# Kernel optimization log

Hardware: AMD Instinct MI355X
Metric: run time of the kernel (lower is better)

The kernel has to match this reference:

```python
import jax, jax.numpy as jnp
import numpy as np
from jax import lax

PAIRS = ((0, 1), (1, 2), (2, 3), (3, 0))


def _apply_1q(state, U, w):
    # state: (N,2,2,2,2); wire w lives at axis w+1
    state = jnp.moveaxis(state, w + 1, -1)
    if U.ndim == 2:  # shared gate across batch
        state = jnp.einsum('ij,...j->...i', U, state)
    else:            # per-batch gate (encoder), U: (N,2,2)
        state = jnp.einsum('nij,n...j->n...i', U, state)
    return jnp.moveaxis(state, -1, w + 1)


def _ry_mat(theta):
    # torchquantum RY: [[cos(t/2), -sin(t/2)], [sin(t/2), cos(t/2)]]
    h = theta * 0.5
    c, s = jnp.cos(h), jnp.sin(h)
    return jnp.stack([jnp.stack([c, -s], -1), jnp.stack([s, c], -1)], -2).astype(jnp.complex64)


def _rz_mat(theta):
    # torchquantum RZ: diag(e^{-i t/2}, e^{+i t/2})
    h = (theta * 0.5).astype(jnp.complex64)
    e0, e1 = jnp.exp(-1j * h), jnp.exp(1j * h)
    z = jnp.zeros_like(e0)
    return jnp.stack([jnp.stack([e0, z], -1), jnp.stack([z, e1], -1)], -2)


def _cnot(state, c, t):
    st = jnp.moveaxis(state, (c + 1, t + 1), (-2, -1))
    st = jnp.stack([st[..., 0, :], st[..., 1, ::-1]], axis=-2)
    return jnp.moveaxis(st, (-2, -1), (c + 1, t + 1))


def _ansatz(state, p, a, b):
    state = _apply_1q(state, _ry_mat(p[0]), a)
    state = _apply_1q(state, _rz_mat(p[1]), a)
    state = _apply_1q(state, _ry_mat(p[2]), b)
    state = _apply_1q(state, _rz_mat(p[3]), b)
    state = _cnot(state, a, b)
    state = _apply_1q(state, _ry_mat(p[4]), a)
    state = _apply_1q(state, _rz_mat(p[5]), a)
    state = _apply_1q(state, _ry_mat(p[6]), b)
    return state


def _circuit(angles, qp):
    # angles: (N,4) in [0,pi]; qp: (2,7). Returns <Z_w> per wire: (N,4)
    N = angles.shape[0]
    state = jnp.zeros((N, 2, 2, 2, 2), jnp.complex64).at[:, 0, 0, 0, 0].set(1.0)
    for w in range(4):  # GeneralEncoder: RY(x_w) on wire w
        state = _apply_1q(state, _ry_mat(angles[:, w]), w)
    for layer in range(2):
        for (a, b) in PAIRS:
            state = _ansatz(state, qp[layer], a, b)
    probs = state.real ** 2 + state.imag ** 2
    exps = []
    for w in range(4):
        axes = tuple(ax for ax in range(1, 5) if ax != w + 1)
        m = probs.sum(axis=axes)  # (N,2)
        exps.append(m[:, 0] - m[:, 1])
    return jnp.stack(exps, axis=-1)


def _conv(x, w, b):
    y = lax.conv_general_dilated(x, w, (1, 1), 'SAME',
                                 dimension_numbers=('NCHW', 'OIHW', 'NCHW'))
    return y + b[None, :, None, None]


def _pool(x):
    return lax.reduce_window(x, -jnp.inf, lax.max, (1, 1, 2, 2), (1, 1, 2, 2), 'VALID')


def setup_inputs() -> dict:
    key = jax.random.key(0)
    ks = jax.random.split(key, 16)
    r = lambda k, sh, sc=0.1: (jax.random.normal(k, sh, dtype=jnp.float32) * sc)
    return {
        'x': jax.random.normal(ks[0], (2048, 1, 28, 28), dtype=jnp.float32),
        'conv1_w': r(ks[1], (64, 1, 3, 3)), 'conv1_b': r(ks[2], (64,)),
        'conv2_w': r(ks[3], (16, 64, 3, 3)), 'conv2_b': r(ks[4], (16,)),
        'conv3_w': r(ks[5], (4, 16, 3, 3)), 'conv3_b': r(ks[6], (4,)),
        'q_params': jax.random.uniform(ks[7], (2, 7), dtype=jnp.float32),
        'fc1_w': r(ks[8], (64, 196)), 'fc1_b': r(ks[9], (64,)),
        'fc2_w': r(ks[10], (128, 64)), 'fc2_b': r(ks[11], (128,)),
        'fc3_w': r(ks[12], (64, 128)), 'fc3_b': r(ks[13], (64,)),
        'fc4_w': r(ks[14], (10, 64)), 'fc4_b': r(ks[15], (10,)),
    }


def reference(x, conv1_w, conv1_b, conv2_w, conv2_b, conv3_w, conv3_b,
              q_params, fc1_w, fc1_b, fc2_w, fc2_b, fc3_w, fc3_b, fc4_w, fc4_b):
    h = _pool(jax.nn.relu(_conv(x, conv1_w, conv1_b)))       # (B,64,14,14)
    h = _pool(jax.nn.relu(_conv(h, conv2_w, conv2_b)))       # (B,16,7,7)
    h = jax.nn.leaky_relu(_conv(h, conv3_w, conv3_b), 0.01)  # (B,4,7,7)
    B, C, H, W = h.shape
    # 1x1 patches: (B, H*W, C) -> flatten over patches
    patches = h.reshape(B, C, H * W).transpose(0, 2, 1).reshape(B * H * W, C)
    angles = jax.nn.sigmoid(patches) * np.float32(np.pi)
    q = _circuit(angles, q_params)            # (B*49, 4)
    q = q.reshape(B, H * W * C)               # (B, 196)
    h = jax.nn.relu(q @ fc1_w.T + fc1_b)
    h = h @ fc2_w.T + fc2_b
    h = jax.nn.relu(h @ fc3_w.T + fc3_b)
    return h @ fc4_w.T + fc4_b
```

## Files before the change

### kernel.cpp

```cpp
#include <hip/hip_runtime.h>
#include <hip/hip_bf16.h>
#include <math.h>

#define DEV __device__ __forceinline__

typedef __attribute__((ext_vector_type(4))) float f32x4;
typedef __attribute__((ext_vector_type(8))) short bf16x8;

DEV unsigned short f2bf(float v) {
    __hip_bfloat16 h = __float2bfloat16(v);
    return *reinterpret_cast<unsigned short*>(&h);
}
DEV unsigned pk2(float a, float b) {
    union { __hip_bfloat162 b2; unsigned u; } cv;
    cv.b2 = __float22bfloat162_rn(float2{a, b});
    return cv.u;
}

template<int B>
DEV void ry_b(float* sr, float* si, float c, float s) {
    #pragma unroll
    for (int i = 0; i < 16; ++i) if (!(i & B)) {
        int j = i | B;
        float r0 = sr[i], m0 = si[i], r1 = sr[j], m1 = si[j];
        sr[i] = c * r0 - s * r1;  si[i] = c * m0 - s * m1;
        sr[j] = s * r0 + c * r1;  si[j] = s * m0 + c * m1;
    }
}
template<int B>
DEV void rz_b(float* sr, float* si, float c, float s) {
    #pragma unroll
    for (int i = 0; i < 16; ++i) {
        float xr = sr[i], xi = si[i];
        if (!(i & B)) { sr[i] = c * xr + s * xi;  si[i] = c * xi - s * xr; }
        else          { sr[i] = c * xr - s * xi;  si[i] = c * xi + s * xr; }
    }
}
template<int BC, int BT>
DEV void cnot_b(float* sr, float* si) {
    #pragma unroll
    for (int i = 0; i < 16; ++i) if ((i & BC) && !(i & BT)) {
        int j = i | BT;
        float tr = sr[i]; sr[i] = sr[j]; sr[j] = tr;
        float ti = si[i]; si[i] = si[j]; si[j] = ti;
    }
}
template<int A, int Bw>
DEV void ansatz(float* sr, float* si, const float* cc, const float* ss) {
    constexpr int BA = 8 >> A, BB = 8 >> Bw;
    ry_b<BA>(sr, si, cc[0], ss[0]);
    rz_b<BA>(sr, si, cc[1], ss[1]);
    ry_b<BB>(sr, si, cc[2], ss[2]);
    rz_b<BB>(sr, si, cc[3], ss[3]);
    cnot_b<BA, BB>(sr, si);
    ry_b<BA>(sr, si, cc[4], ss[4]);
    rz_b<BA>(sr, si, cc[5], ss[5]);
    ry_b<BB>(sr, si, cc[6], ss[6]);
}

__global__ void prep_kernel(const float* __restrict__ w1,
                            const float* __restrict__ w2,
                            const float* __restrict__ w3,
                            const float* __restrict__ qp,
                            const float* __restrict__ fc1w,
                            const float* __restrict__ fc2w,
                            const float* __restrict__ fc3w,
                            const float* __restrict__ fc4w,
                            unsigned short* __restrict__ w1b,
                            unsigned short* __restrict__ w2b,
                            float* __restrict__ w3t,
                            float* __restrict__ ab,
                            float* __restrict__ fc1t,
                            float* __restrict__ fc2t,
                            float* __restrict__ fc3t,
                            float* __restrict__ fc4t)
{
    int t = blockIdx.x * blockDim.x + threadIdx.x;
    int NT = gridDim.x * blockDim.x;
    for (int i = t; i < 2048; i += NT) {
        int j = i & 7, oc = (i >> 3) & 63, fqq = i >> 9;
        int tap = fqq * 8 + j;
        w1b[i] = tap < 9 ? f2bf(w1[oc * 9 + tap]) : (unsigned short)0;
    }
    for (int i = t; i < 9216; i += NT) {
        int j = i & 7, oc = (i >> 3) & 15, fq = (i >> 7) & 3, f = i >> 9;
        int tap = f >> 1, kk = f & 1;
        int s = kk * 32 + fq * 8 + j;
        int ic = (s & 3) * 16 + (s >> 2);
        w2b[i] = f2bf(w2[(oc * 64 + ic) * 9 + tap]);
    }
    for (int i = t; i < 576; i += NT) {
        int c = i & 3, ch = (i >> 2) & 15, tap = i >> 6;
        w3t[i] = w3[(c * 16 + ch) * 9 + tap];
    }
    for (int i = t; i < 12544; i += NT) { int j = i / 196, k = i % 196; fc1t[k * 64 + j] = fc1w[i]; }
    for (int i = t; i < 8192;  i += NT) { int j = i / 64,  k = i % 64;  fc2t[k * 128 + j] = fc2w[i]; }
    for (int i = t; i < 8192;  i += NT) { int j = i / 128, k = i % 128; fc3t[k * 64 + j] = fc3w[i]; }
    for (int i = t; i < 640;   i += NT) { int j = i / 64,  k = i % 64;  fc4t[k * 10 + j] = fc4w[i]; }

    if (blockIdx.x == 0 && threadIdx.x < 16) {
        int b = threadIdx.x;
        float cs0[7], sn0[7], cs1[7], sn1[7];
        #pragma unroll
        for (int k = 0; k < 7; ++k) {
            __sincosf(qp[k] * 0.5f, &sn0[k], &cs0[k]);
            __sincosf(qp[7 + k] * 0.5f, &sn1[k], &cs1[k]);
        }
        float sr[16], si[16];
        #pragma unroll
        for (int i = 0; i < 16; ++i) { sr[i] = (i == b) ? 1.f : 0.f; si[i] = 0.f; }
        ansatz<0, 1>(sr, si, cs0, sn0);
        ansatz<1, 2>(sr, si, cs0, sn0);
        ansatz<2, 3>(sr, si, cs0, sn0);
        ansatz<3, 0>(sr, si, cs0, sn0);
        ansatz<0, 1>(sr, si, cs1, sn1);
        ansatz<1, 2>(sr, si, cs1, sn1);
        ansatz<2, 3>(sr, si, cs1, sn1);
        ansatz<3, 0>(sr, si, cs1, sn1);
        #pragma unroll
        for (int i = 0; i < 16; ++i) {
            ab[(i * 16 + b) * 2]     = sr[i];
            ab[(i * 16 + b) * 2 + 1] = si[i];
        }
    }
}

__global__ __launch_bounds__(256, 3) void conv12_kernel(
    const float* __restrict__ x,
    const float* __restrict__ b1, const unsigned short* __restrict__ w1b,
    const unsigned short* __restrict__ w2b,
    const float* __restrict__ b2, float* __restrict__ out2)
{
    __shared__ __align__(128) char lds_all[36864];
    float* pin = (float*)lds_all;
    char* in_b = lds_all + 4096;
    int t = threadIdx.x, lane = t & 63, wv = t >> 6;
    int fq = lane >> 4, fr = lane & 15;
    int n = blockIdx.x;

    bf16x8 bfrag[18];
    const bf16x8* wb = (const bf16x8*)w2b;
    #pragma unroll
    for (int f = 0; f < 18; ++f) bfrag[f] = wb[(f * 4 + fq) * 16 + fr];
    bf16x8 w1f[4];
    const bf16x8* wb1 = (const bf16x8*)w1b;
    float b1v[4];
    #pragma unroll
    for (int nt = 0; nt < 4; ++nt) {
        w1f[nt] = wb1[fq * 64 + nt * 16 + fr];
        b1v[nt] = b1[nt * 16 + fr];
    }
    float b2v = b2[fr];

    for (int i = t; i < 2048; i += 256) ((f32x4*)in_b)[i] = f32x4{0.f, 0.f, 0.f, 0.f};
    for (int i = t; i < 1020; i += 256) pin[i] = 0.f;
    if (t < 128) {
        int cell = t >> 2, comp = t & 3;
        int pos;
        if (cell < 9)       pos = cell;
        else if (cell < 18) pos = 72 + (cell - 9);
        else if (cell < 25) pos = (cell - 17) * 9;
        else                pos = (cell - 24) * 9 + 8;
        *reinterpret_cast<float4*>(out2 + (size_t)n * 1296 + pos * 16 + comp * 4)
            = float4{0.f, 0.f, 0.f, 0.f};
    }
    __syncthreads();
    for (int i = t; i < 784; i += 256) pin[(i / 28 + 1) * 34 + (i % 28) + 1] = x[n * 784 + i];
    __syncthreads();

    for (int tile = wv; tile < 49; tile += 4) {
        int pooledA = tile * 4 + (fr >> 2);
        int pyA = pooledA / 14, pxA = pooledA - pyA * 14;
        int Y = 2 * pyA + ((fr >> 1) & 1), X = 2 * pxA + (fr & 1);
        const float* ap = pin + Y * 34 + X + (fq == 1 ? 70 : 0);
        float q0 = ap[0],  q1 = ap[1],  q2 = ap[2];
        float q3 = ap[34], q4 = ap[35], q5 = ap[36];
        float q6 = ap[68], q7 = ap[69];
        union { uint4 u; bf16x8 v; } A;
        A.u.x = pk2(q0, q1); A.u.y = pk2(q2, q3);
        A.u.z = pk2(q4, q5); A.u.w = pk2(q6, q7);

        f32x4 a0 = {0.f,0.f,0.f,0.f}, a1 = {0.f,0.f,0.f,0.f},
              a2 = {0.f,0.f,0.f,0.f}, a3 = {0.f,0.f,0.f,0.f};
        a0 = __builtin_amdgcn_mfma_f32_16x16x32_bf16(A.v, w1f[0], a0, 0, 0, 0);
        a1 = __builtin_amdgcn_mfma_f32_16x16x32_bf16(A.v, w1f[1], a1, 0, 0, 0);
        a2 = __builtin_amdgcn_mfma_f32_16x16x32_bf16(A.v, w1f[2], a2, 0, 0, 0);
        a3 = __builtin_amdgcn_mfma_f32_16x16x32_bf16(A.v, w1f[3], a3, 0, 0, 0);

        int pooled = tile * 4 + fq;
        int py = pooled / 14, px = pooled - py * 14;
        int grid = (py + 1) * 16 + (px + 1);
        unsigned swz = (unsigned)(grid & 7) << 4;
        float v0 = fmaxf(fmaxf(fmaxf(a0[0], a0[1]), fmaxf(a0[2], a0[3])) + b1v[0], 0.f);
        float v1 = fmaxf(fmaxf(fmaxf(a1[0], a1[1]), fmaxf(a1[2], a1[3])) + b1v[1], 0.f);
        float v2 = fmaxf(fmaxf(fmaxf(a2[0], a2[1]), fmaxf(a2[2], a2[3])) + b1v[2], 0.f);
        float v3 = fmaxf(fmaxf(fmaxf(a3[0], a3[1]), fmaxf(a3[2], a3[3])) + b1v[3], 0.f);
        uint2 w; w.x = pk2(v0, v1); w.y = pk2(v2, v3);
        *reinterpret_cast<uint2*>(in_b + (((unsigned)grid * 128 + (unsigned)fr * 8) ^ swz)) = w;
    }
    __syncthreads();

    for (int tile = wv; tile < 13; tile += 4) {
        f32x4 acc = {0.f, 0.f, 0.f, 0.f};
        int pv = tile * 4 + (fr >> 2); pv = pv > 48 ? 48 : pv;
        int sub = fr & 3;
        int y7 = pv / 7, x7 = pv - y7 * 7;
        int y = 2 * y7 + (sub >> 1), xx = 2 * x7 + (sub & 1);
        int g0 = y * 16 + xx;
        int vb = g0 * 128 + fq * 16;
        #pragma unroll
        for (int ky = 0; ky < 3; ++ky)
            #pragma unroll
            for (int kx = 0; kx < 3; ++kx) {
                int dg = ky * 16 + kx;
                int msk = ((g0 + dg) & 7) << 4;
                int lin = vb + dg * 128;
                bf16x8 a0 = *(const bf16x8*)(in_b + (lin ^ msk));
                acc = __builtin_amdgcn_mfma_f32_16x16x32_bf16(a0, bfrag[(ky * 3 + kx) * 2], acc, 0, 0, 0);
                bf16x8 a1 = *(const bf16x8*)(in_b + ((lin | 64) ^ msk));
                acc = __builtin_amdgcn_mfma_f32_16x16x32_bf16(a1, bfrag[(ky * 3 + kx) * 2 + 1], acc, 0, 0, 0);
            }
        int pooled2 = tile * 4 + fq;
        if (pooled2 < 49) {
            float m = fmaxf(fmaxf(acc[0], acc[1]), fmaxf(acc[2], acc[3]));
            int y9 = pooled2 / 7, x9 = pooled2 - y9 * 7;
            out2[(size_t)n * 1296 + ((y9 + 1) * 9 + (x9 + 1)) * 16 + fr] =
                fmaxf(m + b2v, 0.f);
        }
    }
}

__global__ __launch_bounds__(256) void qconv_kernel(
    const float* __restrict__ out2, const float* __restrict__ w3t,
    const float* __restrict__ b3, const float* __restrict__ ab,
    float* __restrict__ q)
{
    int gid = blockIdx.x * 256 + threadIdx.x;
    int n = gid / 49, pp = gid % 49;
    int py = pp / 7, px = pp % 7;
    const float* in = out2 + (size_t)n * 1296;

    float acc0 = b3[0], acc1 = b3[1], acc2 = b3[2], acc3 = b3[3];
    #pragma unroll
    for (int ky = 0; ky < 3; ++ky)
        #pragma unroll
        for (int kx = 0; kx < 3; ++kx) {
            const float* cp = in + ((py + ky) * 9 + (px + kx)) * 16;
            const float* wt = w3t + (ky * 3 + kx) * 64;
            #pragma unroll
            for (int icq = 0; icq < 4; ++icq) {
                float4 v4 = *reinterpret_cast<const float4*>(cp + icq * 4);
                const float* wq = wt + icq * 16;
                acc0 = fmaf(wq[0],  v4.x, acc0); acc1 = fmaf(wq[1],  v4.x, acc1);
                acc2 = fmaf(wq[2],  v4.x, acc2); acc3 = fmaf(wq[3],  v4.x, acc3);
                acc0 = fmaf(wq[4],  v4.y, acc0); acc1 = fmaf(wq[5],  v4.y, acc1);
                acc2 = fmaf(wq[6],  v4.y, acc2); acc3 = fmaf(wq[7],  v4.y, acc3);
                acc0 = fmaf(wq[8],  v4.z, acc0); acc1 = fmaf(wq[9],  v4.z, acc1);
                acc2 = fmaf(wq[10], v4.z, acc2); acc3 = fmaf(wq[11], v4.z, acc3);
                acc0 = fmaf(wq[12], v4.w, acc0); acc1 = fmaf(wq[13], v4.w, acc1);
                acc2 = fmaf(wq[14], v4.w, acc2); acc3 = fmaf(wq[15], v4.w, acc3);
            }
        }

    float cw[4], sw[4];
    {
        float az[4] = {acc0, acc1, acc2, acc3};
        #pragma unroll
        for (int c = 0; c < 4; ++c) {
            float z = az[c];
            z = z > 0.f ? z : 0.01f * z;
            float sg = 1.f / (1.f + __expf(-z));
            __sincosf(1.5707963267948966f * sg, &sw[c], &cw[c]);
        }
    }
    float p01[4] = { cw[0]*cw[1], cw[0]*sw[1], sw[0]*cw[1], sw[0]*sw[1] };
    float p23[4] = { cw[2]*cw[3], cw[2]*sw[3], sw[2]*cw[3], sw[2]*sw[3] };
    float v[16];
    #pragma unroll
    for (int i = 0; i < 16; ++i) v[i] = p01[i >> 2] * p23[i & 3];

    float e0 = 0.f, e1 = 0.f, e2 = 0.f, e3 = 0.f;
    #pragma unroll
    for (int i = 0; i < 16; ++i) {
        const float* row = ab + i * 32;
        float re = 0.f, im = 0.f;
        #pragma unroll
        for (int k = 0; k < 16; ++k) {
            re = fmaf(row[k * 2],     v[k], re);
            im = fmaf(row[k * 2 + 1], v[k], im);
        }
        float p = re * re + im * im;
        e0 += (i & 8) ? -p : p;
        e1 += (i & 4) ? -p : p;
        e2 += (i & 2) ? -p : p;
        e3 += (i & 1) ? -p : p;
    }
    float* qo = q + n * 196 + pp * 4;
    qo[0] = e0; qo[1] = e1; qo[2] = e2; qo[3] = e3;
}

__global__ __launch_bounds__(512) void fc_kernel(
    const float* __restrict__ q,
    const float* __restrict__ fc1t, const float* __restrict__ fb1,
    const float* __restrict__ fc2t, const float* __restrict__ fb2,
    const float* __restrict__ fc3t, const float* __restrict__ fb3,
    const float* __restrict__ fc4t, const float* __restrict__ fb4,
    float* __restrict__ out)
{
    __shared__ float qr[8][196], h1[8][64], h2[8][128], h3[8][64];
    int t = threadIdx.x, wv = t >> 6, lane = t & 63;
    int n = blockIdx.x * 8 + wv;
    for (int i = lane; i < 196; i += 64) qr[wv][i] = q[n * 196 + i];
    __syncthreads();
    float a = fb1[lane];
    for (int k = 0; k < 196; ++k) a = fmaf(fc1t[k * 64 + lane], qr[wv][k], a);
    h1[wv][lane] = fmaxf(a, 0.f);
    __syncthreads();
    float a0 = fb2[lane], a1 = fb2[lane + 64];
    for (int k = 0; k < 64; ++k) {
        float v = h1[wv][k];
        a0 = fmaf(fc2t[k * 128 + lane], v, a0);
        a1 = fmaf(fc2t[k * 128 + lane + 64], v, a1);
    }
    h2[wv][lane] = a0; h2[wv][lane + 64] = a1;
    __syncthreads();
    a = fb3[lane];
    for (int k = 0; k < 128; ++k) a = fmaf(fc3t[k * 64 + lane], h2[wv][k], a);
    h3[wv][lane] = fmaxf(a, 0.f);
    __syncthreads();
    if (lane < 10) {
        a = fb4[lane];
        for (int k = 0; k < 64; ++k) a = fmaf(fc4t[k * 10 + lane], h3[wv][k], a);
        out[n * 10 + lane] = a;
    }
}

extern "C" void kernel_launch(void* const* d_in, const int* in_sizes, int n_in,
                              void* d_out, int out_size, void* d_ws, size_t ws_size,
                              hipStream_t stream) {
    const float* x      = (const float*)d_in[0];
    const float* c1w    = (const float*)d_in[1];
    const float* c1b    = (const float*)d_in[2];
    const float* c2w    = (const float*)d_in[3];
    const float* c2b    = (const float*)d_in[4];
    const float* c3w    = (const float*)d_in[5];
    const float* c3b    = (const float*)d_in[6];
    const float* qp     = (const float*)d_in[7];
    const float* fc1w   = (const float*)d_in[8];
    const float* fc1b   = (const float*)d_in[9];
    const float* fc2w   = (const float*)d_in[10];
    const float* fc2b   = (const float*)d_in[11];
    const float* fc3w   = (const float*)d_in[12];
    const float* fc3b   = (const float*)d_in[13];
    const float* fc4w   = (const float*)d_in[14];
    const float* fc4b   = (const float*)d_in[15];
    float* out = (float*)d_out;

    float* ws = (float*)d_ws;
    unsigned short* w2b = (unsigned short*)ws;
    unsigned short* w1b = (unsigned short*)(ws + 4608);
    float* w3t  = ws + 5632;
    float* abm  = ws + 6208;
    float* fc1t = ws + 6720;
    float* fc2t = fc1t + 12544;
    float* fc3t = fc2t + 8192;
    float* fc4t = fc3t + 8192;
    float* out2 = fc4t + 640;
    float* qbuf = out2 + (size_t)2048 * 1296;

    prep_kernel<<<40, 256, 0, stream>>>(c1w, c2w, c3w, qp, fc1w, fc2w, fc3w, fc4w,
                                        w1b, w2b, w3t, abm, fc1t, fc2t, fc3t, fc4t);
    conv12_kernel<<<2048, 256, 0, stream>>>(x, c1b, w1b, w2b, c2b, out2);
    qconv_kernel<<<392, 256, 0, stream>>>(out2, w3t, c3b, abm, qbuf);
    fc_kernel<<<256, 512, 0, stream>>>(qbuf, fc1t, fc1b, fc2t, fc2b,
                                       fc3t, fc3b, fc4t, fc4b, out);
}
```

Measured before the change: 66.72 us.

## Fuse quantum-conv and FC kernels, zero only halo in LDS, raise occupancy

Merges the conv3+quantum-circuit kernel into the FC kernel, so each 512-thread block computes 8 samples' quantum expectations directly into shared memory and drops the global q buffer round trip and one launch. The conv12 kernel now zeroes only the halo border cells of its bf16 input tile instead of the whole 32KB buffer, and its launch bounds ask for 4 blocks per CU instead of 3. The fused kernel runs on only 256 blocks with 392 of 512 threads active in the quantum phase, so parallelism for that stage drops. The higher occupancy target may force register spills in conv12.

```diff
diff --git a/kernel.cpp b/kernel.cpp
--- a/kernel.cpp
+++ b/kernel.cpp
@@ -125,7 +125,7 @@
     }
 }
 
-__global__ __launch_bounds__(256, 3) void conv12_kernel(
+__global__ __launch_bounds__(256, 4) void conv12_kernel(
     const float* __restrict__ x,
     const float* __restrict__ b1, const unsigned short* __restrict__ w1b,
     const unsigned short* __restrict__ w2b,
@@ -152,7 +152,15 @@
     }
     float b2v = b2[fr];
 
-    for (int i = t; i < 2048; i += 256) ((f32x4*)in_b)[i] = f32x4{0.f, 0.f, 0.f, 0.f};
+    for (int i = t; i < 480; i += 256) {
+        int ci = i >> 3, sub = i & 7;
+        int g;
+        if (ci < 16)      g = ci;
+        else if (ci < 32) g = 240 + (ci - 16);
+        else if (ci < 46) g = (ci - 31) * 16;
+        else              g = (ci - 45) * 16 + 15;
+        *(f32x4*)(in_b + g * 128 + sub * 16) = f32x4{0.f, 0.f, 0.f, 0.f};
+    }
     for (int i = t; i < 1020; i += 256) pin[i] = 0.f;
     if (t < 128) {
         int cell = t >> 2, comp = t & 3;
@@ -230,97 +238,96 @@
     }
 }
 
-__global__ __launch_bounds__(256) void qconv_kernel(
+__global__ __launch_bounds__(512) void qfc_kernel(
     const float* __restrict__ out2, const float* __restrict__ w3t,
     const float* __restrict__ b3, const float* __restrict__ ab,
-    float* __restrict__ q)
-{
-    int gid = blockIdx.x * 256 + threadIdx.x;
-    int n = gid / 49, pp = gid % 49;
-    int py = pp / 7, px = pp % 7;
-    const float* in = out2 + (size_t)n * 1296;
-
-    float acc0 = b3[0], acc1 = b3[1], acc2 = b3[2], acc3 = b3[3];
-    #pragma unroll
-    for (int ky = 0; ky < 3; ++ky)
-        #pragma unroll
-        for (int kx = 0; kx < 3; ++kx) {
-            const float* cp = in + ((py + ky) * 9 + (px + kx)) * 16;
-            const float* wt = w3t + (ky * 3 + kx) * 64;
-            #pragma unroll
-            for (int icq = 0; icq < 4; ++icq) {
-                float4 v4 = *reinterpret_cast<const float4*>(cp + icq * 4);
-                const float* wq = wt + icq * 16;
-                acc0 = fmaf(wq[0],  v4.x, acc0); acc1 = fmaf(wq[1],  v4.x, acc1);
-                acc2 = fmaf(wq[2],  v4.x, acc2); acc3 = fmaf(wq[3],  v4.x, acc3);
-                acc0 = fmaf(wq[4],  v4.y, acc0); acc1 = fmaf(wq[5],  v4.y, acc1);
-                acc2 = fmaf(wq[6],  v4.y, acc2); acc3 = fmaf(wq[7],  v4.y, acc3);
-                acc0 = fmaf(wq[8],  v4.z, acc0); acc1 = fmaf(wq[9],  v4.z, acc1);
-                acc2 = fmaf(wq[10], v4.z, acc2); acc3 = fmaf(wq[11], v4.z, acc3);
-                acc0 = fmaf(wq[12], v4.w, acc0); acc1 = fmaf(wq[13], v4.w, acc1);
-                acc2 = fmaf(wq[14], v4.w, acc2); acc3 = fmaf(wq[15], v4.w, acc3);
-            }
-        }
-
-    float cw[4], sw[4];
-    {
-        float az[4] = {acc0, acc1, acc2, acc3};
-        #pragma unroll
-        for (int c = 0; c < 4; ++c) {
-            float z = az[c];
-            z = z > 0.f ? z : 0.01f * z;
-            float sg = 1.f / (1.f + __expf(-z));
-            __sincosf(1.5707963267948966f * sg, &sw[c], &cw[c]);
-        }
-    }
-    float p01[4] = { cw[0]*cw[1], cw[0]*sw[1], sw[0]*cw[1], sw[0]*sw[1] };
-    float p23[4] = { cw[2]*cw[3], cw[2]*sw[3], sw[2]*cw[3], sw[2]*sw[3] };
-    float v[16];
-    #pragma unroll
-    for (int i = 0; i < 16; ++i) v[i] = p01[i >> 2] * p23[i & 3];
-
-    float e0 = 0.f, e1 = 0.f, e2 = 0.f, e3 = 0.f;
-    #pragma unroll
-    for (int i = 0; i < 16; ++i) {
-        const float* row = ab + i * 32;
-        float re = 0.f, im = 0.f;
-        #pragma unroll
-        for (int k = 0; k < 16; ++k) {
-            re = fmaf(row[k * 2],     v[k], re);
-            im = fmaf(row[k * 2 + 1], v[k], im);
-        }
-        float p = re * re + im * im;
-        e0 += (i & 8) ? -p : p;
-        e1 += (i & 4) ? -p : p;
-        e2 += (i & 2) ? -p : p;
-        e3 += (i & 1) ? -p : p;
-    }
-    float* qo = q + n * 196 + pp * 4;
-    qo[0] = e0; qo[1] = e1; qo[2] = e2; qo[3] = e3;
-}
-
-__global__ __launch_bounds__(512) void fc_kernel(
-    const float* __restrict__ q,
     const float* __restrict__ fc1t, const float* __restrict__ fb1,
     const float* __restrict__ fc2t, const float* __restrict__ fb2,
     const float* __restrict__ fc3t, const float* __restrict__ fb3,
     const float* __restrict__ fc4t, const float* __restrict__ fb4,
     float* __restrict__ out)
 {
-    __shared__ float qr[8][196], h1[8][64], h2[8][128], h3[8][64];
-    int t = threadIdx.x, wv = t >> 6, lane = t & 63;
-    int n = blockIdx.x * 8 + wv;
-    for (int i = lane; i < 196; i += 64) qr[wv][i] = q[n * 196 + i];
-    __syncthreads();
+    __shared__ float qr[8][196];
+    __shared__ float h1[8][64], h2[8][128], h3[8][64];
+    int t = threadIdx.x;
+    int nb = blockIdx.x * 8;
+
+    if (t < 392) {
+        int nl = t / 49, p = t - nl * 49;
+        int n = nb + nl;
+        int py = p / 7, px = p - py * 7;
+        const float* in = out2 + (size_t)n * 1296;
+
+        float acc0 = b3[0], acc1 = b3[1], acc2 = b3[2], acc3 = b3[3];
+        #pragma unroll
+        for (int ky = 0; ky < 3; ++ky)
+            #pragma unroll
+            for (int kx = 0; kx < 3; ++kx) {
+                const float* cp = in + ((py + ky) * 9 + (px + kx)) * 16;
+                const float* wt = w3t + (ky * 3 + kx) * 64;
+                #pragma unroll
+                for (int icq = 0; icq < 4; ++icq) {
+                    float4 v4 = *reinterpret_cast<const float4*>(cp + icq * 4);
+                    const float* wq = wt + icq * 16;
+                    acc0 = fmaf(wq[0],  v4.x, acc0); acc1 = fmaf(wq[1],  v4.x, acc1);
+                    acc2 = fmaf(wq[2],  v4.x, acc2); acc3 = fmaf(wq[3],  v4.x, acc3);
+                    acc0 = fmaf(wq[4],  v4.y, acc0); acc1 = fmaf(wq[5],  v4.y, acc1);
+                    acc2 = fmaf(wq[6],  v4.y, acc2); acc3 = fmaf(wq[7],  v4.y, acc3);
+                    acc0 = fmaf(wq[8],  v4.z, acc0); acc1 = fmaf(wq[9],  v4.z, acc1);
+                    acc2 = fmaf(wq[10], v4.z, acc2); acc3 = fmaf(wq[11], v4.z, acc3);
+                    acc0 = fmaf(wq[12], v4.w, acc0); acc1 = fmaf(wq[13], v4.w, acc1);
+                    acc2 = fmaf(wq[14], v4.w, acc2); acc3 = fmaf(wq[15], v4.w, acc3);
+                }
+            }
+
+        float cw[4], sw[4];
+        {
+            float az[4] = {acc0, acc1, acc2, acc3};
+            #pragma unroll
+            for (int c = 0; c < 4; ++c) {
+                float z = az[c];
+                z = z > 0.f ? z : 0.01f * z;
+                float sg = 1.f / (1.f + __expf(-z));
+                __sincosf(1.5707963267948966f * sg, &sw[c], &cw[c]);
+            }
+        }
+        float p01[4] = { cw[0]*cw[1], cw[0]*sw[1], sw[0]*cw[1], sw[0]*sw[1] };
+        float p23[4] = { cw[2]*cw[3], cw[2]*sw[3], sw[2]*cw[3], sw[2]*sw[3] };
+        float v[16];
+        #pragma unroll
+        for (int i = 0; i < 16; ++i) v[i] = p01[i >> 2] * p23[i & 3];
+
+        float e0 = 0.f, e1 = 0.f, e2 = 0.f, e3 = 0.f;
+        #pragma unroll
+        for (int i = 0; i < 16; ++i) {
+            const float* row = ab + i * 32;
+            float re = 0.f, im = 0.f;
+            #pragma unroll
+            for (int k = 0; k < 16; ++k) {
+                re = fmaf(row[k * 2],     v[k], re);
+                im = fmaf(row[k * 2 + 1], v[k], im);
+            }
+            float p2 = re * re + im * im;
+            e0 += (i & 8) ? -p2 : p2;
+            e1 += (i & 4) ? -p2 : p2;
+            e2 += (i & 2) ? -p2 : p2;
+            e3 += (i & 1) ? -p2 : p2;
+        }
+        *reinterpret_cast<float4*>(&qr[nl][p * 4]) = float4{e0, e1, e2, e3};
+    }
+    __syncthreads();
+
+    int wv = t >> 6, lane = t & 63;
+    int n = nb + wv;
     float a = fb1[lane];
     for (int k = 0; k < 196; ++k) a = fmaf(fc1t[k * 64 + lane], qr[wv][k], a);
     h1[wv][lane] = fmaxf(a, 0.f);
     __syncthreads();
     float a0 = fb2[lane], a1 = fb2[lane + 64];
     for (int k = 0; k < 64; ++k) {
-        float v = h1[wv][k];
-        a0 = fmaf(fc2t[k * 128 + lane], v, a0);
-        a1 = fmaf(fc2t[k * 128 + lane + 64], v, a1);
+        float vv = h1[wv][k];
+        a0 = fmaf(fc2t[k * 128 + lane], vv, a0);
+        a1 = fmaf(fc2t[k * 128 + lane + 64], vv, a1);
     }
     h2[wv][lane] = a0; h2[wv][lane + 64] = a1;
     __syncthreads();
@@ -366,12 +373,11 @@
     float* fc3t = fc2t + 8192;
     float* fc4t = fc3t + 8192;
     float* out2 = fc4t + 640;
-    float* qbuf = out2 + (size_t)2048 * 1296;
 
     prep_kernel<<<40, 256, 0, stream>>>(c1w, c2w, c3w, qp, fc1w, fc2w, fc3w, fc4w,
                                         w1b, w2b, w3t, abm, fc1t, fc2t, fc3t, fc4t);
     conv12_kernel<<<2048, 256, 0, stream>>>(x, c1b, w1b, w2b, c2b, out2);
-    qconv_kernel<<<392, 256, 0, stream>>>(out2, w3t, c3b, abm, qbuf);
-    fc_kernel<<<256, 512, 0, stream>>>(qbuf, fc1t, fc1b, fc2t, fc2b,
-                                       fc3t, fc3b, fc4t, fc4b, out);
-}
+    qfc_kernel<<<256, 512, 0, stream>>>(out2, w3t, c3b, abm,
+                                        fc1t, fc1b, fc2t, fc2b,
+                                        fc3t, fc3b, fc4t, fc4b, out);
+}
```

Measured after the change: 63.81 us. 4.4% less time.
